# Kernel tuning notes

Hardware: AMD Instinct MI355X
Metric: run time of the kernel (lower is better)

Reference implementation:

```python
import jax, jax.numpy as jnp
import numpy as np

N = 100000   # nodes
E = 800000   # edges (avg degree ~8)
G = 64       # graphs in batch
F_IN = 64
H = 128
C = 4


def setup_inputs() -> dict:
    key = jax.random.key(0)
    ks = jax.random.split(key, 14)
    def w(k, fin, fout):
        return jax.random.normal(k, (fin, fout), dtype=jnp.float32) * (1.0 / np.sqrt(fin))
    inp = {
        "x": jax.random.normal(ks[0], (N, F_IN), dtype=jnp.float32),
        "W1": w(ks[1], F_IN, H), "b1": jnp.zeros((H,), jnp.float32),
        "W2": w(ks[2], H, H),    "b2": jnp.zeros((H,), jnp.float32),
        "W3": w(ks[3], H, H),    "b3": jnp.zeros((H,), jnp.float32),
        "fw1": w(ks[4], H, H),   "fb1": jnp.zeros((H,), jnp.float32),
        "fw2": w(ks[5], H, C),   "fb2": jnp.zeros((C,), jnp.float32),
        "edge_index": jax.random.randint(ks[6], (2, E), 0, N, dtype=jnp.int32),
        "batch": jnp.sort(jax.random.randint(ks[7], (N,), 0, G, dtype=jnp.int32)),
    }
    return inp


def gcn_conv(x, W, b, src, dst):
    """PyG GCNConv: linear transform, add self-loops, symmetric deg^-1/2 norm, scatter-add."""
    h = x @ W                                                    # [N, H]
    deg = jax.ops.segment_sum(jnp.ones((E,), x.dtype), dst, num_segments=N) + 1.0  # self-loop
    dinv = jax.lax.rsqrt(deg)                                    # [N]
    norm = dinv[src] * dinv[dst]                                 # [E]
    agg = jax.ops.segment_sum(h[src] * norm[:, None], dst, num_segments=N)
    agg = agg + h * (dinv * dinv)[:, None]                       # self-loop term (norm = 1/deg)
    return agg + b


def reference(x, W1, b1, W2, b2, W3, b3, fw1, fb1, fw2, fb2, edge_index, batch):
    src, dst = edge_index[0], edge_index[1]
    h = jax.nn.relu(gcn_conv(x, W1, b1, src, dst))
    h = jax.nn.relu(gcn_conv(h, W2, b2, src, dst))
    h = gcn_conv(h, W3, b3, src, dst)
    # global mean pool over graphs
    s = jax.ops.segment_sum(h, batch, num_segments=G)            # [G, H]
    cnt = jax.ops.segment_sum(jnp.ones((N,), h.dtype), batch, num_segments=G)
    pooled = s / jnp.maximum(cnt, 1.0)[:, None]
    z = jax.nn.relu(pooled @ fw1 + fb1)
    return z @ fw2 + fb2                                          # [G, C]
```

## Files before the change

### kernel.cpp

```cpp
#include <hip/hip_runtime.h>

#define N_NODES 100000
#define N_EDGES 800000
#define G_GRAPHS 64
#define F_INPUT 64
#define H_DIM 128
#define C_OUT 4
#define SCAN_BLOCKS ((N_NODES + 255) / 256)
#define FILL_SEG 8
#define FILL_CHUNKS 125
#define FILL_RANGE (N_NODES / FILL_SEG)
#define FILL_CHUNK (N_EDGES / FILL_CHUNKS)

typedef __attribute__((ext_vector_type(8))) short bf16x8;
typedef __attribute__((ext_vector_type(8))) unsigned short u16x8;
typedef __attribute__((ext_vector_type(4))) float f32x4;

__device__ inline unsigned short f2bf(float f) {
    union { float f; unsigned int u; } v; v.f = f;
    unsigned int u = v.u + 0x7FFFu + ((v.u >> 16) & 1u);
    return (unsigned short)(u >> 16);
}
__device__ inline float bf2f(unsigned short b) {
    union { unsigned int u; float f; } v; v.u = ((unsigned int)b) << 16;
    return v.f;
}
__device__ inline float2 unpack_pair(unsigned int u) {
    union { unsigned int u; float f; } a, b;
    a.u = u << 16; b.u = u & 0xFFFF0000u;
    float2 r; r.x = a.f; r.y = b.f; return r;
}
__device__ inline unsigned char f2fp8(float v) {
    int r = __builtin_amdgcn_cvt_pk_fp8_f32(v, 0.0f, 0, false);
    return (unsigned char)(r & 0xFF);
}

__global__ void hist_kernel(const int* __restrict__ dst, int* __restrict__ cnt,
                            int* __restrict__ slot) {
    int e = blockIdx.x * 256 + threadIdx.x;
    if (e < N_EDGES) slot[e] = atomicAdd(&cnt[dst[e]], 1);
}
__global__ __launch_bounds__(256) void scan1_kernel(
    const int* __restrict__ cnt, int* __restrict__ pre, int* __restrict__ bsum)
{
    __shared__ int tmp[256];
    int i = blockIdx.x * 256 + threadIdx.x;
    int v = (i < N_NODES) ? cnt[i] : 0;
    tmp[threadIdx.x] = v;
    __syncthreads();
    for (int off = 1; off < 256; off <<= 1) {
        int t = (threadIdx.x >= off) ? tmp[threadIdx.x - off] : 0;
        __syncthreads();
        tmp[threadIdx.x] += t;
        __syncthreads();
    }
    if (i < N_NODES) pre[i] = tmp[threadIdx.x] - v;
    if (threadIdx.x == 255) bsum[blockIdx.x] = tmp[255];
}
__global__ __launch_bounds__(256) void scan3x_kernel(
    const int* __restrict__ pre, const int* __restrict__ bsum,
    const int* __restrict__ cnt, const float4* __restrict__ x4,
    int* __restrict__ offs, float* __restrict__ dinv, unsigned int* __restrict__ xb_u)
{
    __shared__ int red[256];
    __shared__ float dl[256];
    int partial = 0;
    for (int j = threadIdx.x; j < blockIdx.x; j += 256) partial += bsum[j];
    red[threadIdx.x] = partial;
    __syncthreads();
    for (int off = 128; off > 0; off >>= 1) {
        if (threadIdx.x < off) red[threadIdx.x] += red[threadIdx.x + off];
        __syncthreads();
    }
    const int base = red[0];

    int i = blockIdx.x * 256 + threadIdx.x;
    float dv = 0.0f;
    if (i < N_NODES) {
        offs[i] = pre[i] + base;
        dv = rsqrtf((float)cnt[i] + 1.0f);
        dinv[i] = dv;
    }
    if (i == 0) offs[N_NODES] = N_EDGES;
    dl[threadIdx.x] = dv;
    __syncthreads();
    const int row_base = blockIdx.x * 256;
    for (int c = threadIdx.x; c < 256 * 16; c += 256) {
        int r = c >> 4;
        int row = row_base + r;
        if (row < N_NODES) {
            float d2 = dl[r];
            float4 v = x4[(size_t)row * 16 + (c & 15)];
            size_t o = ((size_t)row * 16 + (c & 15)) * 2;
            xb_u[o + 0] = (unsigned int)f2bf(v.x * d2) | ((unsigned int)f2bf(v.y * d2) << 16);
            xb_u[o + 1] = (unsigned int)f2bf(v.z * d2) | ((unsigned int)f2bf(v.w * d2) << 16);
        }
    }
}
__global__ __launch_bounds__(256) void fill_kernel(
    const int* __restrict__ src, const int* __restrict__ dst,
    const int* __restrict__ offs, const int* __restrict__ slot,
    int* __restrict__ csr)
{
    const int r  = blockIdx.x & (FILL_SEG - 1);
    const int m  = blockIdx.x >> 3;
    const int lo = r * FILL_RANGE;
    const int hi = lo + FILL_RANGE;
    const int e0 = m * FILL_CHUNK;
    for (int e = e0 + threadIdx.x; e < e0 + FILL_CHUNK; e += 256) {
        int d = dst[e];
        if (d >= lo && d < hi)
            csr[offs[d] + slot[e]] = src[e];
    }
}

__device__ inline void wpack_one(const float* __restrict__ W, unsigned short* __restrict__ hi,
                                 unsigned short* __restrict__ lo, int K, int t)
{
    int lane = t & 63;
    int tile = t >> 6;
    int KS = K / 32;
    int ct = tile / KS, ks = tile % KS;
    int n  = ct * 16 + (lane & 15);
    int k0 = ks * 32 + (lane >> 4) * 8;
    #pragma unroll
    for (int j = 0; j < 8; j++) {
        float w = W[(k0 + j) * H_DIM + n];
        unsigned short h = f2bf(w);
        hi[t * 8 + j] = h;
        lo[t * 8 + j] = f2bf(w - bf2f(h));
    }
}
__global__ __launch_bounds__(256) void wpack_all_kernel(
    const float* __restrict__ W1, const float* __restrict__ W2, const float* __restrict__ W3,
    unsigned short* __restrict__ w1hi, unsigned short* __restrict__ w1lo,
    unsigned short* __restrict__ w2hi, unsigned short* __restrict__ w2lo,
    unsigned short* __restrict__ w3hi, unsigned short* __restrict__ w3lo)
{
    int t = blockIdx.x * 256 + threadIdx.x;
    if (t < 1024)       wpack_one(W1, w1hi, w1lo, F_INPUT, t);
    else if (t < 3072)  wpack_one(W2, w2hi, w2lo, H_DIM, t - 1024);
    else if (t < 5120)  wpack_one(W3, w3hi, w3lo, H_DIM, t - 3072);
}

template <int K, bool BIAS_RELU, bool OUT_FP8>
__global__ __launch_bounds__(256) void mfma_gemm_kernel(
    const unsigned short* __restrict__ in, const unsigned short* __restrict__ whi,
    const unsigned short* __restrict__ wlo, const float* __restrict__ dinv,
    const float* __restrict__ bias, void* __restrict__ outv)
{
    constexpr int KS = K / 32;
    __shared__ unsigned short As[128 * K];

    const int tid  = threadIdx.x;
    const int row0 = blockIdx.x * 128;

    const int CH = 128 * K / 8;
    for (int c = tid; c < CH; c += 256) {
        int mt   = c / (KS * 64);
        int rest = c % (KS * 64);
        int ks   = rest / 64;
        int ln   = rest % 64;
        int r    = mt * 16 + (ln & 15);
        int k    = ks * 32 + (ln >> 4) * 8;
        int gr   = row0 + r; if (gr >= N_NODES) gr = N_NODES - 1;
        *(u16x8*)(As + c * 8) = *(const u16x8*)(in + (size_t)gr * K + k);
    }
    __syncthreads();

    const int w = tid >> 6, lane = tid & 63;
    const int quad = lane >> 4, l16 = lane & 15;

    f32x4 acc[2][8];
    #pragma unroll
    for (int rt = 0; rt < 2; rt++)
        #pragma unroll
        for (int ct = 0; ct < 8; ct++) acc[rt][ct] = (f32x4)(0.0f);

    #pragma unroll
    for (int ks = 0; ks < KS; ks++) {
        bf16x8 a0 = *(const bf16x8*)(As + (((w * 2 + 0) * KS + ks) * 64 + lane) * 8);
        bf16x8 a1 = *(const bf16x8*)(As + (((w * 2 + 1) * KS + ks) * 64 + lane) * 8);
        bf16x8 bh[8], bl[8];
        #pragma unroll
        for (int ct = 0; ct < 8; ct++) {
            bh[ct] = *(const bf16x8*)(whi + ((size_t)(ct * KS + ks) * 64 + lane) * 8);
            bl[ct] = *(const bf16x8*)(wlo + ((size_t)(ct * KS + ks) * 64 + lane) * 8);
        }
        #pragma unroll
        for (int ct = 0; ct < 8; ct++) {
            acc[0][ct] = __builtin_amdgcn_mfma_f32_16x16x32_bf16(a0, bh[ct], acc[0][ct], 0, 0, 0);
            acc[0][ct] = __builtin_amdgcn_mfma_f32_16x16x32_bf16(a0, bl[ct], acc[0][ct], 0, 0, 0);
            acc[1][ct] = __builtin_amdgcn_mfma_f32_16x16x32_bf16(a1, bh[ct], acc[1][ct], 0, 0, 0);
            acc[1][ct] = __builtin_amdgcn_mfma_f32_16x16x32_bf16(a1, bl[ct], acc[1][ct], 0, 0, 0);
        }
    }

    float bv[8];
    if (BIAS_RELU) {
        #pragma unroll
        for (int ct = 0; ct < 8; ct++) bv[ct] = bias[ct * 16 + l16];
    }

    #pragma unroll
    for (int rt = 0; rt < 2; rt++) {
        #pragma unroll
        for (int reg = 0; reg < 4; reg++) {
            int row = row0 + w * 32 + rt * 16 + quad * 4 + reg;
            if (row < N_NODES) {
                if (BIAS_RELU) {
                    unsigned short* out = (unsigned short*)outv;
                    #pragma unroll
                    for (int ct = 0; ct < 8; ct++)
                        out[(size_t)row * H_DIM + ct * 16 + l16] =
                            f2bf(fmaxf(acc[rt][ct][reg] + bv[ct], 0.0f));
                } else if (OUT_FP8) {
                    unsigned char* out = (unsigned char*)outv;
                    float dv = dinv[row];
                    #pragma unroll
                    for (int ct = 0; ct < 8; ct++)
                        out[(size_t)row * H_DIM + ct * 16 + l16] = f2fp8(acc[rt][ct][reg] * dv);
                } else {
                    unsigned short* out = (unsigned short*)outv;
                    float dv = dinv[row];
                    #pragma unroll
                    for (int ct = 0; ct < 8; ct++)
                        out[(size_t)row * H_DIM + ct * 16 + l16] = f2bf(acc[rt][ct][reg] * dv);
                }
            }
        }
    }
}

template <int SHIFT, bool RELU, bool BIAS>
__global__ __launch_bounds__(256) void gather_kernel(
    const unsigned int* __restrict__ hs_u, const int* __restrict__ offs,
    const int* __restrict__ csr, const float* __restrict__ dinv,
    const float* __restrict__ bias, unsigned int* __restrict__ outb)
{
    const int F2 = 1 << SHIFT;
    int idx = blockIdx.x * 256 + threadIdx.x;
    int i  = idx >> SHIFT;
    int f2 = idx & (F2 - 1);
    int beg = offs[i];
    int end = offs[i + 1];
    float2 acc = unpack_pair(hs_u[(size_t)i * F2 + f2]);
    int e = beg;
    while (e + 8 <= end) {
        int s0 = csr[e+0], s1 = csr[e+1], s2 = csr[e+2], s3 = csr[e+3];
        int s4 = csr[e+4], s5 = csr[e+5], s6 = csr[e+6], s7 = csr[e+7];
        float2 v0 = unpack_pair(hs_u[(size_t)s0 * F2 + f2]);
        float2 v1 = unpack_pair(hs_u[(size_t)s1 * F2 + f2]);
        float2 v2 = unpack_pair(hs_u[(size_t)s2 * F2 + f2]);
        float2 v3 = unpack_pair(hs_u[(size_t)s3 * F2 + f2]);
        float2 v4 = unpack_pair(hs_u[(size_t)s4 * F2 + f2]);
        float2 v5 = unpack_pair(hs_u[(size_t)s5 * F2 + f2]);
        float2 v6 = unpack_pair(hs_u[(size_t)s6 * F2 + f2]);
        float2 v7 = unpack_pair(hs_u[(size_t)s7 * F2 + f2]);
        acc.x += ((v0.x + v1.x) + (v2.x + v3.x)) + ((v4.x + v5.x) + (v6.x + v7.x));
        acc.y += ((v0.y + v1.y) + (v2.y + v3.y)) + ((v4.y + v5.y) + (v6.y + v7.y));
        e += 8;
    }
    if (e + 4 <= end) {
        int s0 = csr[e+0], s1 = csr[e+1], s2 = csr[e+2], s3 = csr[e+3];
        float2 v0 = unpack_pair(hs_u[(size_t)s0 * F2 + f2]);
        float2 v1 = unpack_pair(hs_u[(size_t)s1 * F2 + f2]);
        float2 v2 = unpack_pair(hs_u[(size_t)s2 * F2 + f2]);
        float2 v3 = unpack_pair(hs_u[(size_t)s3 * F2 + f2]);
        acc.x += (v0.x + v1.x) + (v2.x + v3.x);
        acc.y += (v0.y + v1.y) + (v2.y + v3.y);
        e += 4;
    }
    while (e < end) {
        int s = csr[e++];
        float2 v = unpack_pair(hs_u[(size_t)s * F2 + f2]);
        acc.x += v.x; acc.y += v.y;
    }
    float dv = dinv[i];
    float vx = acc.x * dv;
    float vy = acc.y * dv;
    if (BIAS) {
        float2 bvv = *(const float2*)(bias + f2 * 2);
        vx += bvv.x; vy += bvv.y;
    }
    if (RELU) { vx = fmaxf(vx, 0.0f); vy = fmaxf(vy, 0.0f); }
    outb[idx] = (unsigned int)f2bf(vx) | ((unsigned int)f2bf(vy) << 16);
}

template <bool RELU>
__global__ __launch_bounds__(256) void gather_fp8_kernel(
    const unsigned int* __restrict__ hs8, const int* __restrict__ offs,
    const int* __restrict__ csr, const float* __restrict__ dinv,
    const float* __restrict__ bias, unsigned int* __restrict__ outb)
{
    int idx = blockIdx.x * 256 + threadIdx.x;
    int i  = idx >> 5;
    int f4 = idx & 31;
    const unsigned int* base = hs8 + f4;
    int beg = offs[i];
    int end = offs[i + 1];

    float a0 = 0.0f, a1 = 0.0f, a2 = 0.0f, a3 = 0.0f;
    {
        unsigned int w = base[(size_t)i * 32];
        auto lo = __builtin_amdgcn_cvt_pk_f32_fp8(w, false);
        auto hi = __builtin_amdgcn_cvt_pk_f32_fp8(w, true);
        a0 += lo[0]; a1 += lo[1]; a2 += hi[0]; a3 += hi[1];
    }
    int e = beg;
    while (e + 8 <= end) {
        unsigned int w0 = base[(size_t)csr[e+0] * 32];
        unsigned int w1 = base[(size_t)csr[e+1] * 32];
        unsigned int w2 = base[(size_t)csr[e+2] * 32];
        unsigned int w3 = base[(size_t)csr[e+3] * 32];
        unsigned int w4 = base[(size_t)csr[e+4] * 32];
        unsigned int w5 = base[(size_t)csr[e+5] * 32];
        unsigned int w6 = base[(size_t)csr[e+6] * 32];
        unsigned int w7 = base[(size_t)csr[e+7] * 32];
        #pragma unroll
        for (unsigned int w : {w0, w1, w2, w3, w4, w5, w6, w7}) {
            auto lo = __builtin_amdgcn_cvt_pk_f32_fp8(w, false);
            auto hi = __builtin_amdgcn_cvt_pk_f32_fp8(w, true);
            a0 += lo[0]; a1 += lo[1]; a2 += hi[0]; a3 += hi[1];
        }
        e += 8;
    }
    if (e + 4 <= end) {
        unsigned int w0 = base[(size_t)csr[e+0] * 32];
        unsigned int w1 = base[(size_t)csr[e+1] * 32];
        unsigned int w2 = base[(size_t)csr[e+2] * 32];
        unsigned int w3 = base[(size_t)csr[e+3] * 32];
        #pragma unroll
        for (unsigned int w : {w0, w1, w2, w3}) {
            auto lo = __builtin_amdgcn_cvt_pk_f32_fp8(w, false);
            auto hi = __builtin_amdgcn_cvt_pk_f32_fp8(w, true);
            a0 += lo[0]; a1 += lo[1]; a2 += hi[0]; a3 += hi[1];
        }
        e += 4;
    }
    while (e < end) {
        unsigned int w = base[(size_t)csr[e++] * 32];
        auto lo = __builtin_amdgcn_cvt_pk_f32_fp8(w, false);
        auto hi = __builtin_amdgcn_cvt_pk_f32_fp8(w, true);
        a0 += lo[0]; a1 += lo[1]; a2 += hi[0]; a3 += hi[1];
    }

    float dv = dinv[i];
    float4 bv = *(const float4*)(bias + f4 * 4);
    float v0 = a0 * dv + bv.x;
    float v1 = a1 * dv + bv.y;
    float v2 = a2 * dv + bv.z;
    float v3 = a3 * dv + bv.w;
    if (RELU) {
        v0 = fmaxf(v0, 0.0f); v1 = fmaxf(v1, 0.0f);
        v2 = fmaxf(v2, 0.0f); v3 = fmaxf(v3, 0.0f);
    }
    uint2 o;
    o.x = (unsigned int)f2bf(v0) | ((unsigned int)f2bf(v1) << 16);
    o.y = (unsigned int)f2bf(v2) | ((unsigned int)f2bf(v3) << 16);
    *(uint2*)(outb + (size_t)i * 64 + f4 * 2) = o;
}

__global__ __launch_bounds__(128) void pool_kernel(
    const unsigned short* __restrict__ A, const int* __restrict__ batch,
    float* __restrict__ s, float* __restrict__ cnt)
{
    const int RPB = 32;
    int row0 = blockIdx.x * RPB;
    int f = threadIdx.x;
    int g0 = batch[row0];
    int g1 = batch[row0 + RPB - 1];
    if (g0 == g1) {
        float acc = 0.0f;
        #pragma unroll
        for (int r = 0; r < RPB; r++)
            acc += bf2f(A[(size_t)(row0 + r) * H_DIM + f]);
        unsafeAtomicAdd(&s[g0 * H_DIM + f], acc);
        if (f == 0) unsafeAtomicAdd(&cnt[g0], (float)RPB);
    } else {
        float acc = 0.0f;
        int cur = g0, c = 0;
        for (int r = 0; r < RPB; r++) {
            int g = batch[row0 + r];
            if (g != cur) {
                unsafeAtomicAdd(&s[cur * H_DIM + f], acc);
                if (f == 0) unsafeAtomicAdd(&cnt[cur], (float)c);
                cur = g; acc = 0.0f; c = 0;
            }
            acc += bf2f(A[(size_t)(row0 + r) * H_DIM + f]);
            c++;
        }
        unsafeAtomicAdd(&s[cur * H_DIM + f], acc);
        if (f == 0) unsafeAtomicAdd(&cnt[cur], (float)c);
    }
}

__global__ __launch_bounds__(128) void mlp_kernel(
    const float* __restrict__ s, const float* __restrict__ cnt,
    const float* __restrict__ fw1, const float* __restrict__ fb1,
    const float* __restrict__ fw2, const float* __restrict__ fb2,
    float* __restrict__ out)
{
    __shared__ float p[H_DIM];
    __shared__ float z[H_DIM];
    int g = blockIdx.x;
    int f = threadIdx.x;
    float c = fmaxf(cnt[g], 1.0f);
    p[f] = s[g * H_DIM + f] / c;
    __syncthreads();
    float acc = fb1[f];
    for (int k = 0; k < H_DIM; k++) acc = fmaf(p[k], fw1[k * H_DIM + f], acc);
    z[f] = fmaxf(acc, 0.0f);
    __syncthreads();
    if (f < C_OUT) {
        float o = fb2[f];
        for (int k = 0; k < H_DIM; k++) o = fmaf(z[k], fw2[k * C_OUT + f], o);
        out[g * C_OUT + f] = o;
    }
}

extern "C" void kernel_launch(void* const* d_in, const int* in_sizes, int n_in,
                              void* d_out, int out_size, void* d_ws, size_t ws_size,
                              hipStream_t stream)
{
    const float* x   = (const float*)d_in[0];
    const float* W1  = (const float*)d_in[1];
    const float* b1  = (const float*)d_in[2];
    const float* W2  = (const float*)d_in[3];
    const float* b2  = (const float*)d_in[4];
    const float* W3  = (const float*)d_in[5];
    const float* b3  = (const float*)d_in[6];
    const float* fw1 = (const float*)d_in[7];
    const float* fb1 = (const float*)d_in[8];
    const float* fw2 = (const float*)d_in[9];
    const float* fb2 = (const float*)d_in[10];
    const int*   ei  = (const int*)d_in[11];
    const int*   bat = (const int*)d_in[12];
    const int* esrc = ei;
    const int* edst = ei + N_EDGES;
    float* out = (float*)d_out;

    char* ws = (char*)d_ws;
    unsigned short* bufA = (unsigned short*)ws;  ws += (size_t)N_NODES * H_DIM * 2;
    unsigned short* bufB = (unsigned short*)ws;  ws += (size_t)N_NODES * H_DIM * 2;
    unsigned char*  buf8 = (unsigned char*)ws;   ws += (size_t)N_NODES * H_DIM;
    unsigned short* xb   = (unsigned short*)ws;  ws += (size_t)N_NODES * F_INPUT * 2;
    unsigned short* w1hi = (unsigned short*)ws;  ws += H_DIM * F_INPUT * 2;
    unsigned short* w1lo = (unsigned short*)ws;  ws += H_DIM * F_INPUT * 2;
    unsigned short* w2hi = (unsigned short*)ws;  ws += H_DIM * H_DIM * 2;
    unsigned short* w2lo = (unsigned short*)ws;  ws += H_DIM * H_DIM * 2;
    unsigned short* w3hi = (unsigned short*)ws;  ws += H_DIM * H_DIM * 2;
    unsigned short* w3lo = (unsigned short*)ws;  ws += H_DIM * H_DIM * 2;
    float* dinv = (float*)ws;  ws += N_NODES * 4;
    float* s    = (float*)ws;  ws += G_GRAPHS * H_DIM * 4;
    float* cnt  = (float*)ws;  ws += G_GRAPHS * 4;
    int* cnti   = (int*)ws;    ws += N_NODES * 4;
    int* pre    = (int*)ws;    ws += N_NODES * 4;
    int* offs   = (int*)ws;    ws += (N_NODES + 1) * 4;
    int* bsum   = (int*)ws;    ws += (SCAN_BLOCKS + 1) * 4;
    int* slot   = (int*)ws;    ws += (size_t)N_EDGES * 4;
    int* csr    = (int*)ws;    ws += (size_t)N_EDGES * 4;

    hipMemsetAsync(cnti, 0, N_NODES * sizeof(int), stream);
    hipMemsetAsync(s, 0, (G_GRAPHS * H_DIM + G_GRAPHS) * sizeof(float), stream);

    const int egrid = (N_EDGES + 255) / 256;
    hist_kernel<<<egrid, 256, 0, stream>>>(edst, cnti, slot);
    scan1_kernel<<<SCAN_BLOCKS, 256, 0, stream>>>(cnti, pre, bsum);
    scan3x_kernel<<<SCAN_BLOCKS, 256, 0, stream>>>(
        pre, bsum, cnti, (const float4*)x, offs, dinv, (unsigned int*)xb);
    fill_kernel<<<FILL_SEG * FILL_CHUNKS, 256, 0, stream>>>(esrc, edst, offs, slot, csr);

    wpack_all_kernel<<<20, 256, 0, stream>>>(W1, W2, W3, w1hi, w1lo, w2hi, w2lo, w3hi, w3lo);

    const int gemm_grid = (N_NODES + 127) / 128;
    const int gath_grid64 = (N_NODES * 32) / 256;
    const int gath_grid8  = (N_NODES * 32) / 256;

    gather_kernel<5, false, false><<<gath_grid64, 256, 0, stream>>>(
        (const unsigned int*)xb, offs, csr, dinv, nullptr, (unsigned int*)bufA);
    mfma_gemm_kernel<64, true, false><<<gemm_grid, 256, 0, stream>>>(
        bufA, w1hi, w1lo, dinv, b1, bufB);
    mfma_gemm_kernel<128, false, true><<<gemm_grid, 256, 0, stream>>>(
        bufB, w2hi, w2lo, dinv, nullptr, buf8);
    gather_fp8_kernel<true><<<gath_grid8, 256, 0, stream>>>(
        (const unsigned int*)buf8, offs, csr, dinv, b2, (unsigned int*)bufA);
    mfma_gemm_kernel<128, false, true><<<gemm_grid, 256, 0, stream>>>(
        bufA, w3hi, w3lo, dinv, nullptr, buf8);
    gather_fp8_kernel<false><<<gath_grid8, 256, 0, stream>>>(
        (const unsigned int*)buf8, offs, csr, dinv, b3, (unsigned int*)bufB);

    pool_kernel<<<N_NODES / 32, 128, 0, stream>>>(bufB, bat, s, cnt);
    mlp_kernel<<<G_GRAPHS, 128, 0, stream>>>(s, cnt, fw1, fb1, fw2, fb2, out);
}
```

Measured before the change: 347.8 us.

## Store intermediate activations in fp8 and fuse final gather with mean pooling

```diff
diff --git a/kernel.cpp b/kernel.cpp
--- a/kernel.cpp
+++ b/kernel.cpp
@@ -143,9 +143,9 @@
     else if (t < 5120)  wpack_one(W3, w3hi, w3lo, H_DIM, t - 3072);
 }
 
-template <int K, bool BIAS_RELU, bool OUT_FP8>
+template <int K, bool BIAS_RELU, bool IN_FP8, bool OUT_FP8>
 __global__ __launch_bounds__(256) void mfma_gemm_kernel(
-    const unsigned short* __restrict__ in, const unsigned short* __restrict__ whi,
+    const void* __restrict__ inv, const unsigned short* __restrict__ whi,
     const unsigned short* __restrict__ wlo, const float* __restrict__ dinv,
     const float* __restrict__ bias, void* __restrict__ outv)
 {
@@ -164,7 +164,23 @@
         int r    = mt * 16 + (ln & 15);
         int k    = ks * 32 + (ln >> 4) * 8;
         int gr   = row0 + r; if (gr >= N_NODES) gr = N_NODES - 1;
-        *(u16x8*)(As + c * 8) = *(const u16x8*)(in + (size_t)gr * K + k);
+        if constexpr (IN_FP8) {
+            const unsigned char* in8 = (const unsigned char*)inv;
+            uint2 t = *(const uint2*)(in8 + (size_t)gr * K + k);
+            auto f0 = __builtin_amdgcn_cvt_pk_f32_fp8(t.x, false);
+            auto f1 = __builtin_amdgcn_cvt_pk_f32_fp8(t.x, true);
+            auto f2 = __builtin_amdgcn_cvt_pk_f32_fp8(t.y, false);
+            auto f3 = __builtin_amdgcn_cvt_pk_f32_fp8(t.y, true);
+            u16x8 v;
+            v[0] = f2bf(f0[0]); v[1] = f2bf(f0[1]);
+            v[2] = f2bf(f1[0]); v[3] = f2bf(f1[1]);
+            v[4] = f2bf(f2[0]); v[5] = f2bf(f2[1]);
+            v[6] = f2bf(f3[0]); v[7] = f2bf(f3[1]);
+            *(u16x8*)(As + c * 8) = v;
+        } else {
+            const unsigned short* in16 = (const unsigned short*)inv;
+            *(u16x8*)(As + c * 8) = *(const u16x8*)(in16 + (size_t)gr * K + k);
+        }
     }
     __syncthreads();
 
@@ -208,39 +224,31 @@
         for (int reg = 0; reg < 4; reg++) {
             int row = row0 + w * 32 + rt * 16 + quad * 4 + reg;
             if (row < N_NODES) {
-                if (BIAS_RELU) {
-                    unsigned short* out = (unsigned short*)outv;
-                    #pragma unroll
-                    for (int ct = 0; ct < 8; ct++)
-                        out[(size_t)row * H_DIM + ct * 16 + l16] =
-                            f2bf(fmaxf(acc[rt][ct][reg] + bv[ct], 0.0f));
-                } else if (OUT_FP8) {
-                    unsigned char* out = (unsigned char*)outv;
-                    float dv = dinv[row];
-                    #pragma unroll
-                    for (int ct = 0; ct < 8; ct++)
-                        out[(size_t)row * H_DIM + ct * 16 + l16] = f2fp8(acc[rt][ct][reg] * dv);
-                } else {
-                    unsigned short* out = (unsigned short*)outv;
-                    float dv = dinv[row];
-                    #pragma unroll
-                    for (int ct = 0; ct < 8; ct++)
-                        out[(size_t)row * H_DIM + ct * 16 + l16] = f2bf(acc[rt][ct][reg] * dv);
+                float dv = BIAS_RELU ? 0.0f : dinv[row];
+                #pragma unroll
+                for (int ct = 0; ct < 8; ct++) {
+                    float val;
+                    if (BIAS_RELU) val = fmaxf(acc[rt][ct][reg] + bv[ct], 0.0f);
+                    else           val = acc[rt][ct][reg] * dv;
+                    if constexpr (OUT_FP8) {
+                        ((unsigned char*)outv)[(size_t)row * H_DIM + ct * 16 + l16] = f2fp8(val);
+                    } else {
+                        ((unsigned short*)outv)[(size_t)row * H_DIM + ct * 16 + l16] = f2bf(val);
+                    }
                 }
             }
         }
     }
 }
 
-template <int SHIFT, bool RELU, bool BIAS>
-__global__ __launch_bounds__(256) void gather_kernel(
+__global__ __launch_bounds__(256) void gather_bf16_kernel(
     const unsigned int* __restrict__ hs_u, const int* __restrict__ offs,
     const int* __restrict__ csr, const float* __restrict__ dinv,
-    const float* __restrict__ bias, unsigned int* __restrict__ outb)
-{
-    const int F2 = 1 << SHIFT;
+    unsigned int* __restrict__ outb)
+{
+    const int F2 = 32;
     int idx = blockIdx.x * 256 + threadIdx.x;
-    int i  = idx >> SHIFT;
+    int i  = idx >> 5;
     int f2 = idx & (F2 - 1);
     int beg = offs[i];
     int end = offs[i + 1];
@@ -277,30 +285,13 @@
         acc.x += v.x; acc.y += v.y;
     }
     float dv = dinv[i];
-    float vx = acc.x * dv;
-    float vy = acc.y * dv;
-    if (BIAS) {
-        float2 bvv = *(const float2*)(bias + f2 * 2);
-        vx += bvv.x; vy += bvv.y;
-    }
-    if (RELU) { vx = fmaxf(vx, 0.0f); vy = fmaxf(vy, 0.0f); }
-    outb[idx] = (unsigned int)f2bf(vx) | ((unsigned int)f2bf(vy) << 16);
-}
-
-template <bool RELU>
-__global__ __launch_bounds__(256) void gather_fp8_kernel(
-    const unsigned int* __restrict__ hs8, const int* __restrict__ offs,
-    const int* __restrict__ csr, const float* __restrict__ dinv,
-    const float* __restrict__ bias, unsigned int* __restrict__ outb)
-{
-    int idx = blockIdx.x * 256 + threadIdx.x;
-    int i  = idx >> 5;
-    int f4 = idx & 31;
-    const unsigned int* base = hs8 + f4;
-    int beg = offs[i];
-    int end = offs[i + 1];
-
-    float a0 = 0.0f, a1 = 0.0f, a2 = 0.0f, a3 = 0.0f;
+    outb[idx] = (unsigned int)f2bf(acc.x * dv) | ((unsigned int)f2bf(acc.y * dv) << 16);
+}
+
+__device__ inline void gather_fp8_acc(
+    const unsigned int* __restrict__ base, const int* __restrict__ csr,
+    int i, int beg, int end, float& a0, float& a1, float& a2, float& a3)
+{
     {
         unsigned int w = base[(size_t)i * 32];
         auto lo = __builtin_amdgcn_cvt_pk_f32_fp8(w, false);
@@ -344,54 +335,70 @@
         auto hi = __builtin_amdgcn_cvt_pk_f32_fp8(w, true);
         a0 += lo[0]; a1 += lo[1]; a2 += hi[0]; a3 += hi[1];
     }
-
+}
+
+__global__ __launch_bounds__(256) void gather_fp8_kernel(
+    const unsigned int* __restrict__ hs8, const int* __restrict__ offs,
+    const int* __restrict__ csr, const float* __restrict__ dinv,
+    const float* __restrict__ bias, unsigned int* __restrict__ out8)
+{
+    int idx = blockIdx.x * 256 + threadIdx.x;
+    int i  = idx >> 5;
+    int f4 = idx & 31;
+    const unsigned int* base = hs8 + f4;
+    float a0 = 0, a1 = 0, a2 = 0, a3 = 0;
+    gather_fp8_acc(base, csr, i, offs[i], offs[i + 1], a0, a1, a2, a3);
+    float dv = dinv[i];
+    float4 bv = *(const float4*)(bias + f4 * 4);
+    float v0 = fmaxf(a0 * dv + bv.x, 0.0f);
+    float v1 = fmaxf(a1 * dv + bv.y, 0.0f);
+    float v2 = fmaxf(a2 * dv + bv.z, 0.0f);
+    float v3 = fmaxf(a3 * dv + bv.w, 0.0f);
+    int d = __builtin_amdgcn_cvt_pk_fp8_f32(v0, v1, 0, false);
+    d = __builtin_amdgcn_cvt_pk_fp8_f32(v2, v3, d, true);
+    out8[(size_t)i * 32 + f4] = (unsigned int)d;
+}
+
+__global__ __launch_bounds__(256) void gather3_pool_kernel(
+    const unsigned int* __restrict__ hs8, const int* __restrict__ offs,
+    const int* __restrict__ csr, const float* __restrict__ dinv,
+    const float* __restrict__ bias, const int* __restrict__ batch,
+    float* __restrict__ s, float* __restrict__ cnt)
+{
+    __shared__ float sl[H_DIM];
+    const int tid = threadIdx.x;
+    if (tid < H_DIM) sl[tid] = 0.0f;
+    __syncthreads();
+
+    int i  = blockIdx.x * 8 + (tid >> 5);
+    int f4 = tid & 31;
+    const unsigned int* base = hs8 + f4;
+    float a0 = 0, a1 = 0, a2 = 0, a3 = 0;
+    gather_fp8_acc(base, csr, i, offs[i], offs[i + 1], a0, a1, a2, a3);
     float dv = dinv[i];
     float4 bv = *(const float4*)(bias + f4 * 4);
     float v0 = a0 * dv + bv.x;
     float v1 = a1 * dv + bv.y;
     float v2 = a2 * dv + bv.z;
     float v3 = a3 * dv + bv.w;
-    if (RELU) {
-        v0 = fmaxf(v0, 0.0f); v1 = fmaxf(v1, 0.0f);
-        v2 = fmaxf(v2, 0.0f); v3 = fmaxf(v3, 0.0f);
-    }
-    uint2 o;
-    o.x = (unsigned int)f2bf(v0) | ((unsigned int)f2bf(v1) << 16);
-    o.y = (unsigned int)f2bf(v2) | ((unsigned int)f2bf(v3) << 16);
-    *(uint2*)(outb + (size_t)i * 64 + f4 * 2) = o;
-}
-
-__global__ __launch_bounds__(128) void pool_kernel(
-    const unsigned short* __restrict__ A, const int* __restrict__ batch,
-    float* __restrict__ s, float* __restrict__ cnt)
-{
-    const int RPB = 32;
-    int row0 = blockIdx.x * RPB;
-    int f = threadIdx.x;
-    int g0 = batch[row0];
-    int g1 = batch[row0 + RPB - 1];
-    if (g0 == g1) {
-        float acc = 0.0f;
-        #pragma unroll
-        for (int r = 0; r < RPB; r++)
-            acc += bf2f(A[(size_t)(row0 + r) * H_DIM + f]);
-        unsafeAtomicAdd(&s[g0 * H_DIM + f], acc);
-        if (f == 0) unsafeAtomicAdd(&cnt[g0], (float)RPB);
+
+    int g0 = batch[blockIdx.x * 8];
+    int g7 = batch[blockIdx.x * 8 + 7];
+    if (g0 == g7) {
+        atomicAdd(&sl[f4 * 4 + 0], v0);
+        atomicAdd(&sl[f4 * 4 + 1], v1);
+        atomicAdd(&sl[f4 * 4 + 2], v2);
+        atomicAdd(&sl[f4 * 4 + 3], v3);
+        __syncthreads();
+        if (tid < H_DIM) unsafeAtomicAdd(&s[g0 * H_DIM + tid], sl[tid]);
+        if (tid == 0) unsafeAtomicAdd(&cnt[g0], 8.0f);
     } else {
-        float acc = 0.0f;
-        int cur = g0, c = 0;
-        for (int r = 0; r < RPB; r++) {
-            int g = batch[row0 + r];
-            if (g != cur) {
-                unsafeAtomicAdd(&s[cur * H_DIM + f], acc);
-                if (f == 0) unsafeAtomicAdd(&cnt[cur], (float)c);
-                cur = g; acc = 0.0f; c = 0;
-            }
-            acc += bf2f(A[(size_t)(row0 + r) * H_DIM + f]);
-            c++;
-        }
-        unsafeAtomicAdd(&s[cur * H_DIM + f], acc);
-        if (f == 0) unsafeAtomicAdd(&cnt[cur], (float)c);
+        int g = batch[i];
+        unsafeAtomicAdd(&s[g * H_DIM + f4 * 4 + 0], v0);
+        unsafeAtomicAdd(&s[g * H_DIM + f4 * 4 + 1], v1);
+        unsafeAtomicAdd(&s[g * H_DIM + f4 * 4 + 2], v2);
+        unsafeAtomicAdd(&s[g * H_DIM + f4 * 4 + 3], v3);
+        if (f4 == 0) unsafeAtomicAdd(&cnt[g], 1.0f);
     }
 }
 
@@ -441,10 +448,11 @@
     float* out = (float*)d_out;
 
     char* ws = (char*)d_ws;
-    unsigned short* bufA = (unsigned short*)ws;  ws += (size_t)N_NODES * H_DIM * 2;
-    unsigned short* bufB = (unsigned short*)ws;  ws += (size_t)N_NODES * H_DIM * 2;
-    unsigned char*  buf8 = (unsigned char*)ws;   ws += (size_t)N_NODES * H_DIM;
     unsigned short* xb   = (unsigned short*)ws;  ws += (size_t)N_NODES * F_INPUT * 2;
+    unsigned short* aggA = (unsigned short*)ws;  ws += (size_t)N_NODES * F_INPUT * 2;
+    unsigned char*  p0   = (unsigned char*)ws;   ws += (size_t)N_NODES * H_DIM;
+    unsigned char*  p1   = (unsigned char*)ws;   ws += (size_t)N_NODES * H_DIM;
+    unsigned char*  p2   = (unsigned char*)ws;   ws += (size_t)N_NODES * H_DIM;
     unsigned short* w1hi = (unsigned short*)ws;  ws += H_DIM * F_INPUT * 2;
     unsigned short* w1lo = (unsigned short*)ws;  ws += H_DIM * F_INPUT * 2;
     unsigned short* w2hi = (unsigned short*)ws;  ws += H_DIM * H_DIM * 2;
@@ -452,17 +460,16 @@
     unsigned short* w3hi = (unsigned short*)ws;  ws += H_DIM * H_DIM * 2;
     unsigned short* w3lo = (unsigned short*)ws;  ws += H_DIM * H_DIM * 2;
     float* dinv = (float*)ws;  ws += N_NODES * 4;
-    float* s    = (float*)ws;  ws += G_GRAPHS * H_DIM * 4;
-    float* cnt  = (float*)ws;  ws += G_GRAPHS * 4;
-    int* cnti   = (int*)ws;    ws += N_NODES * 4;
     int* pre    = (int*)ws;    ws += N_NODES * 4;
     int* offs   = (int*)ws;    ws += (N_NODES + 1) * 4;
     int* bsum   = (int*)ws;    ws += (SCAN_BLOCKS + 1) * 4;
     int* slot   = (int*)ws;    ws += (size_t)N_EDGES * 4;
     int* csr    = (int*)ws;    ws += (size_t)N_EDGES * 4;
-
-    hipMemsetAsync(cnti, 0, N_NODES * sizeof(int), stream);
-    hipMemsetAsync(s, 0, (G_GRAPHS * H_DIM + G_GRAPHS) * sizeof(float), stream);
+    int*   cnti = (int*)ws;    ws += N_NODES * 4;
+    float* s    = (float*)ws;  ws += G_GRAPHS * H_DIM * 4;
+    float* cnt  = (float*)ws;  ws += G_GRAPHS * 4;
+
+    hipMemsetAsync(cnti, 0, (N_NODES + G_GRAPHS * H_DIM + G_GRAPHS) * sizeof(int), stream);
 
     const int egrid = (N_EDGES + 255) / 256;
     hist_kernel<<<egrid, 256, 0, stream>>>(edst, cnti, slot);
@@ -474,22 +481,20 @@
     wpack_all_kernel<<<20, 256, 0, stream>>>(W1, W2, W3, w1hi, w1lo, w2hi, w2lo, w3hi, w3lo);
 
     const int gemm_grid = (N_NODES + 127) / 128;
-    const int gath_grid64 = (N_NODES * 32) / 256;
-    const int gath_grid8  = (N_NODES * 32) / 256;
-
-    gather_kernel<5, false, false><<<gath_grid64, 256, 0, stream>>>(
-        (const unsigned int*)xb, offs, csr, dinv, nullptr, (unsigned int*)bufA);
-    mfma_gemm_kernel<64, true, false><<<gemm_grid, 256, 0, stream>>>(
-        bufA, w1hi, w1lo, dinv, b1, bufB);
-    mfma_gemm_kernel<128, false, true><<<gemm_grid, 256, 0, stream>>>(
-        bufB, w2hi, w2lo, dinv, nullptr, buf8);
-    gather_fp8_kernel<true><<<gath_grid8, 256, 0, stream>>>(
-        (const unsigned int*)buf8, offs, csr, dinv, b2, (unsigned int*)bufA);
-    mfma_gemm_kernel<128, false, true><<<gemm_grid, 256, 0, stream>>>(
-        bufA, w3hi, w3lo, dinv, nullptr, buf8);
-    gather_fp8_kernel<false><<<gath_grid8, 256, 0, stream>>>(
-        (const unsigned int*)buf8, offs, csr, dinv, b3, (unsigned int*)bufB);
-
-    pool_kernel<<<N_NODES / 32, 128, 0, stream>>>(bufB, bat, s, cnt);
+    const int gath_grid = (N_NODES * 32) / 256;
+
+    gather_bf16_kernel<<<gath_grid, 256, 0, stream>>>(
+        (const unsigned int*)xb, offs, csr, dinv, (unsigned int*)aggA);
+    mfma_gemm_kernel<64, true, false, true><<<gemm_grid, 256, 0, stream>>>(
+        aggA, w1hi, w1lo, dinv, b1, p0);
+    mfma_gemm_kernel<128, false, true, true><<<gemm_grid, 256, 0, stream>>>(
+        p0, w2hi, w2lo, dinv, nullptr, p1);
+    gather_fp8_kernel<<<gath_grid, 256, 0, stream>>>(
+        (const unsigned int*)p1, offs, csr, dinv, b2, (unsigned int*)p2);
+    mfma_gemm_kernel<128, false, true, true><<<gemm_grid, 256, 0, stream>>>(
+        p2, w3hi, w3lo, dinv, nullptr, p0);
+    gather3_pool_kernel<<<N_NODES / 8, 256, 0, stream>>>(
+        (const unsigned int*)p0, offs, csr, dinv, b3, bat, s, cnt);
+
     mlp_kernel<<<G_GRAPHS, 128, 0, stream>>>(s, cnt, fw1, fb1, fw2, fb2, out);
 }
```

Result: slower. 423.1 us (+21.6%).
